# Kernel tuning notes

Hardware: AMD Instinct MI355X
Metric: run time of the kernel (lower is better)

Reference implementation:

```python
import jax, jax.numpy as jnp
import numpy as np

N_P, N_V, N_C, N_A = 8000, 3000, 1500, 6000
CLS = N_C
D = 128
E = 150000
N_TOT = N_P + N_V + N_C + N_A
LAMBDA1 = 1.0


def _cal_matrix(A):
    # row-normalize, leaving all-zero rows untouched (matches cal_matrix)
    d = jnp.sum(A, axis=1)
    safe = jnp.where(d > 0, d, 1.0)
    return jnp.where((d > 0)[:, None], A / safe[:, None], A)


def _linear(x, W, b):
    return x @ W.T + b


def _gru(x, h, Wih, Whh, bih, bhh):
    # torch.nn.GRUCell semantics; gate order r, z, n
    gi = x @ Wih.T + bih
    gh = h @ Whh.T + bhh
    ir, iz, inn = jnp.split(gi, 3, axis=1)
    hr, hz, hn = jnp.split(gh, 3, axis=1)
    r = jax.nn.sigmoid(ir + hr)
    z = jax.nn.sigmoid(iz + hz)
    n = jnp.tanh(inn + r * hn)
    return (1.0 - z) * n + z * h


def _ce_soft(pred, label):
    # torch CrossEntropyLoss with probabilistic targets; NOTE: pred is already
    # softmaxed in the original, so log_softmax is applied on top (faithful double softmax)
    return -jnp.mean(jnp.sum(label * jax.nn.log_softmax(pred, axis=1), axis=1))


def _fuse(e0, e1, W2, b2, W3, b3):
    # attention fusion: leaky_relu(., 0) == relu; softmax over the NODE axis (faithful)
    a = jnp.concatenate([_linear(e0, W2, b2), _linear(e1, W3, b3)], axis=0)  # [2N,1]
    alpha = jax.nn.softmax(jax.nn.relu(a).reshape(2, -1, 1), axis=1)
    return jax.nn.relu(jnp.sum(alpha * jnp.stack([e0, e1], axis=0), axis=0))


def _forward(feat_P, feat_V, feat_C, feat_A, W1, b1, W2, b2, W3, b3,
             L00W, L00b, L01W, L01b, L10W, L10b, L11W, L11b, L12W, L12b,
             g0_Wih, g0_Whh, g0_bih, g0_bhh, g1_Wih, g1_Whh, g1_bih, g1_bhh,
             rel_emb, adj00, adj01, adj10, adj11, adj12, clsA, clsP, clsV, u_s, u_d):
    # self embeddings via shared linear1
    self_P = _linear(feat_P, W1, b1)
    self_V = _linear(feat_V, W1, b1)
    self_C = _linear(feat_C, W1, b1)
    self_A = _linear(feat_A, W1, b1)
    loss_tcp = jnp.float32(0.0)
    # ---- meta-path 0: V -> P -> A (GRUCell 0) ----
    pred = jax.nn.softmax(_linear(feat_V, L00W, L00b), axis=1)        # [N_V, CLS]
    loss_tcp += _ce_soft(pred, clsV)
    tcp = jnp.sum(pred * clsV, axis=1, keepdims=True)                 # bmm([N,1,C],[N,C,1])
    h = adj00 @ (tcp * feat_V)                                        # [N_P, D]
    state_P0 = _gru(feat_P, h, g0_Wih, g0_Whh, g0_bih, g0_bhh)
    pred = jax.nn.softmax(_linear(state_P0, L01W, L01b), axis=1)
    loss_tcp += _ce_soft(pred, clsP)
    tcp = jnp.sum(pred * clsP, axis=1, keepdims=True)
    h = adj01 @ (tcp * state_P0)                                      # [N_A, D]
    state_A0 = _gru(feat_A, h, g0_Wih, g0_Whh, g0_bih, g0_bhh)
    # ---- meta-path 1: A -> P -> V -> C (GRUCell 1) ----
    pred = jax.nn.softmax(_linear(feat_A, L10W, L10b), axis=1)
    loss_tcp += _ce_soft(pred, clsA)
    tcp = jnp.sum(pred * clsA, axis=1, keepdims=True)
    h = adj10 @ (tcp * feat_A)                                        # [N_P, D]
    state_P1 = _gru(feat_P, h, g1_Wih, g1_Whh, g1_bih, g1_bhh)        # appended 3rd, unused by fusion
    pred = jax.nn.softmax(_linear(state_P1, L11W, L11b), axis=1)
    loss_tcp += _ce_soft(pred, clsP)
    tcp = jnp.sum(pred * clsP, axis=1, keepdims=True)
    h = adj11 @ (tcp * state_P1)                                      # [N_V, D]
    state_V1 = _gru(feat_V, h, g1_Wih, g1_Whh, g1_bih, g1_bhh)
    pred = jax.nn.softmax(_linear(state_V1, L12W, L12b), axis=1)
    loss_tcp += _ce_soft(pred, clsV)
    tcp = jnp.sum(pred * clsV, axis=1, keepdims=True)
    h = adj12 @ (tcp * state_V1)                                      # [N_C, D]
    state_C1 = _gru(feat_C, h, g1_Wih, g1_Whh, g1_bih, g1_bhh)
    # ---- attention fusion of (self_emb, first GRU state) per node type ----
    emb_P = _fuse(self_P, state_P0, W2, b2, W3, b3)
    emb_V = _fuse(self_V, state_V1, W2, b2, W3, b3)
    emb_C = _fuse(self_C, state_C1, W2, b2, W3, b3)
    emb_A = _fuse(self_A, state_A0, W2, b2, W3, b3)
    final_ent = jnp.concatenate([emb_P, emb_V, emb_C, emb_A], axis=0)  # order P,V,C,A
    # ---- link scoring ----
    lab_d = u_d[:, 2].astype(jnp.float32)
    lab_s = u_s[:, 2].astype(jnp.float32)
    M_r = rel_emb[u_d[:, 3]]
    inner_d = jnp.sum(M_r * jnp.tanh(final_ent[u_d[:, 0]] + final_ent[u_d[:, 1]]), axis=1)
    inner_s = jnp.sum(final_ent[u_s[:, 0]] * final_ent[u_s[:, 1]], axis=1)
    base = -jnp.sum(jax.nn.log_sigmoid(lab_d * inner_d)) - jnp.sum(jax.nn.log_sigmoid(lab_s * inner_s))
    # l2_loss_emb is 0 in the original; l2_loss is computed but never added to loss_emb
    loss = base + LAMBDA1 * loss_tcp
    return loss, final_ent, rel_emb


def setup_inputs():
    key = jax.random.key(0)
    ki = iter(jax.random.split(key, 48))
    def nk():
        return next(ki)
    def xav(o, i):  # xavier_normal_
        return jax.random.normal(nk(), (o, i), jnp.float32) * jnp.sqrt(2.0 / (o + i))
    def uni(shape):  # torch GRUCell default init
        k = 1.0 / float(np.sqrt(D))
        return jax.random.uniform(nk(), shape, jnp.float32, -k, k)
    def radj(o, i, p=0.003):  # raw binary adjacency
        return (jax.random.uniform(nk(), (o, i)) < p).astype(jnp.float32)

    feat_P = jax.random.normal(nk(), (N_P, D), jnp.float32)
    feat_V = jax.random.normal(nk(), (N_V, D), jnp.float32)
    feat_C = jax.random.normal(nk(), (N_C, D), jnp.float32)
    feat_A = jax.random.normal(nk(), (N_A, D), jnp.float32)
    A00 = radj(N_P, N_V); A01 = radj(N_A, N_P)
    A10 = radj(N_P, N_A); A11 = radj(N_V, N_P); A12 = radj(N_C, N_V)

    inp = dict(
        feat_P=feat_P, feat_V=feat_V, feat_C=feat_C, feat_A=feat_A,
        W1=xav(D, D), b1=jnp.zeros((D,), jnp.float32),
        W2=xav(1, D), b2=jnp.zeros((1,), jnp.float32),
        W3=xav(1, D), b3=jnp.zeros((1,), jnp.float32),
        L00W=xav(CLS, D), L00b=jnp.zeros((CLS,), jnp.float32),
        L01W=xav(CLS, D), L01b=jnp.zeros((CLS,), jnp.float32),
        L10W=xav(CLS, D), L10b=jnp.zeros((CLS,), jnp.float32),
        L11W=xav(CLS, D), L11b=jnp.zeros((CLS,), jnp.float32),
        L12W=xav(CLS, D), L12b=jnp.zeros((CLS,), jnp.float32),
        g0_Wih=uni((3 * D, D)), g0_Whh=uni((3 * D, D)), g0_bih=uni((3 * D,)), g0_bhh=uni((3 * D,)),
        g1_Wih=uni((3 * D, D)), g1_Whh=uni((3 * D, D)), g1_bih=uni((3 * D,)), g1_bhh=uni((3 * D,)),
        rel_emb=jax.random.normal(nk(), (12, D), jnp.float32),
        adj00=_cal_matrix(A00), adj01=_cal_matrix(A01),
        adj10=_cal_matrix(A10), adj11=_cal_matrix(A11), adj12=_cal_matrix(A12),
        clsA=_cal_matrix((A12 @ (A11 @ A10)).T),   # [N_A, CLS]
        clsP=_cal_matrix((A12 @ A11).T),           # [N_P, CLS]
        clsV=_cal_matrix(A12.T),                   # [N_V, CLS]
    )

    def edges(n_cols):
        i = jax.random.randint(nk(), (E,), 0, N_TOT)
        j = jax.random.randint(nk(), (E,), 0, N_TOT)
        lab = jax.random.randint(nk(), (E,), 0, 2) * 2 - 1  # labels in {-1,+1}
        cols = [i, j, lab]
        if n_cols == 4:
            cols.append(jax.random.randint(nk(), (E,), 0, 12))
        return jnp.stack(cols, axis=1)

    inp['u_s'] = edges(3)
    inp['u_d'] = edges(4)
    return inp


def reference(feat_P, feat_V, feat_C, feat_A, W1, b1, W2, b2, W3, b3,
              L00W, L00b, L01W, L01b, L10W, L10b, L11W, L11b, L12W, L12b,
              g0_Wih, g0_Whh, g0_bih, g0_bhh, g1_Wih, g1_Whh, g1_bih, g1_bhh,
              rel_emb, adj00, adj01, adj10, adj11, adj12, clsA, clsP, clsV, u_s, u_d):
    return _forward(feat_P, feat_V, feat_C, feat_A, W1, b1, W2, b2, W3, b3,
                    L00W, L00b, L01W, L01b, L10W, L10b, L11W, L11b, L12W, L12b,
                    g0_Wih, g0_Whh, g0_bih, g0_bhh, g1_Wih, g1_Whh, g1_bih, g1_bhh,
                    rel_emb, adj00, adj01, adj10, adj11, adj12, clsA, clsP, clsV, u_s, u_d)
```

## Files before the change

### kernel.cpp

```cpp
#include <hip/hip_runtime.h>
#include <cstdint>
#include <cstddef>

#define DEV_INLINE __device__ __forceinline__

typedef __attribute__((ext_vector_type(8))) short bf16x8;
typedef __attribute__((ext_vector_type(16))) float f32x16;
struct __align__(8) US4 { unsigned short u[4]; };

DEV_INLINE unsigned short f2bf(float x) {
  unsigned u = __float_as_uint(x);
  return (unsigned short)((u + 0x7FFFu + ((u >> 16) & 1u)) >> 16);
}
DEV_INLINE float2 bfpair(unsigned v) {
  return make_float2(__uint_as_float(v << 16), __uint_as_float(v & 0xFFFF0000u));
}

struct CvtSeg { const float* src; unsigned short* dst; int n; int nblk; };
struct CvtArgs { CvtSeg seg[16]; int nseg; };

__global__ __launch_bounds__(256) void convert_bf16_many(CvtArgs args) {
  int b = blockIdx.x;
  int s = 0;
  while (s < args.nseg && b >= args.seg[s].nblk) { b -= args.seg[s].nblk; ++s; }
  if (s >= args.nseg) return;
  int base = b * 1024 + threadIdx.x * 4;
  if (base >= args.seg[s].n) return;
  float4 v = *reinterpret_cast<const float4*>(args.seg[s].src + base);
  US4 o;
  o.u[0] = f2bf(v.x); o.u[1] = f2bf(v.y); o.u[2] = f2bf(v.z); o.u[3] = f2bf(v.w);
  *reinterpret_cast<US4*>(args.seg[s].dst + base) = o;
}

DEV_INLINE void gemm_body(
    const unsigned short* __restrict__ Xb, const unsigned short* __restrict__ Wb,
    const float* __restrict__ bias, float* __restrict__ C, int N, int O,
    int bm, int bn, unsigned short* Xs, unsigned short* Ws)
{
  const int tid = threadIdx.x;
#pragma unroll
  for (int i = 0; i < 8; ++i) {
    int s = tid + 256 * i;
    int row = s >> 4, c16 = s & 15;
    uint4 v = make_uint4(0, 0, 0, 0);
    int gr = bm + row;
    if (gr < N) v = *reinterpret_cast<const uint4*>(Xb + (size_t)gr * 128 + c16 * 8);
    *reinterpret_cast<uint4*>(&Xs[(row * 16 + (c16 ^ (row & 7))) * 8]) = v;
  }
#pragma unroll
  for (int i = 0; i < 4; ++i) {
    int s = tid + 256 * i;
    int row = s >> 4, c16 = s & 15;
    uint4 v = make_uint4(0, 0, 0, 0);
    int gw = bn + row;
    if (gw < O) v = *reinterpret_cast<const uint4*>(Wb + (size_t)gw * 128 + c16 * 8);
    *reinterpret_cast<uint4*>(&Ws[(row * 16 + (c16 ^ (row & 7))) * 8]) = v;
  }
  __syncthreads();

  const int wave = tid >> 6, lane = tid & 63;
  const int l31 = lane & 31, lhi = lane >> 5;

  f32x16 acc0, acc1;
#pragma unroll
  for (int i = 0; i < 16; ++i) { acc0[i] = 0.f; acc1[i] = 0.f; }

  const int ar = wave * 32 + l31;
#pragma unroll
  for (int ks = 0; ks < 8; ++ks) {
    int c16 = ks * 2 + lhi;
    bf16x8 a  = *reinterpret_cast<const bf16x8*>(&Xs[(ar * 16 + (c16 ^ (ar & 7))) * 8]);
    bf16x8 b0 = *reinterpret_cast<const bf16x8*>(&Ws[(l31 * 16 + (c16 ^ (l31 & 7))) * 8]);
    int br1 = 32 + l31;
    bf16x8 b1 = *reinterpret_cast<const bf16x8*>(&Ws[(br1 * 16 + (c16 ^ (br1 & 7))) * 8]);
    acc0 = __builtin_amdgcn_mfma_f32_32x32x16_bf16(a, b0, acc0, 0, 0, 0);
    acc1 = __builtin_amdgcn_mfma_f32_32x32x16_bf16(a, b1, acc1, 0, 0, 0);
  }

#pragma unroll
  for (int reg = 0; reg < 16; ++reg) {
    int r = bm + wave * 32 + (reg & 3) + 8 * (reg >> 2) + 4 * lhi;
    if (r < N) {
      int c0 = bn + l31;
      if (c0 < O) C[(size_t)r * O + c0] = acc0[reg] + bias[c0];
      int c1 = bn + 32 + l31;
      if (c1 < O) C[(size_t)r * O + c1] = acc1[reg] + bias[c1];
    }
  }
}

__global__ __launch_bounds__(256) void gemm_bf16(
    const unsigned short* __restrict__ Xb, const unsigned short* __restrict__ Wb,
    const float* __restrict__ bias, float* __restrict__ C, int N, int O)
{
  __shared__ __align__(16) unsigned short Xs[128 * 128];
  __shared__ __align__(16) unsigned short Ws[64 * 128];
  gemm_body(Xb, Wb, bias, C, N, O, blockIdx.x * 128, blockIdx.y * 64, Xs, Ws);
}

struct GSeg { const unsigned short* X; const unsigned short* W; const float* bias;
              float* C; int N; int O; int blk0; int xblk; };
struct GSegs { GSeg s[8]; int nseg; };

__global__ __launch_bounds__(256) void gemm_bf16_gseg(GSegs gs) {
  __shared__ __align__(16) unsigned short Xs[128 * 128];
  __shared__ __align__(16) unsigned short Ws[64 * 128];
  int bx = blockIdx.x;
  int si = 0;
  while (si + 1 < gs.nseg && bx >= gs.s[si + 1].blk0) ++si;
  const GSeg& g = gs.s[si];
  int b = bx - g.blk0;
  int bm = (b % g.xblk) * 128;
  int bn = (b / g.xblk) * 64;
  gemm_body(g.X, g.W, g.bias, g.C, g.N, g.O, bm, bn, Xs, Ws);
}

DEV_INLINE void ghgru_body(
    const unsigned short* __restrict__ Hb, const unsigned short* __restrict__ Whhb,
    const float* __restrict__ bhh, const float* __restrict__ gi,
    const float* __restrict__ hv, float* __restrict__ out,
    unsigned short* __restrict__ outb, int M, int bm, unsigned short* As)
{
  const int tid = threadIdx.x;
#pragma unroll
  for (int i = 0; i < 2; ++i) {
    int s = tid + 256 * i;
    int row = s >> 4, c16 = s & 15;
    uint4 v = make_uint4(0, 0, 0, 0);
    int gr = bm + row;
    if (gr < M) v = *reinterpret_cast<const uint4*>(Hb + (size_t)gr * 128 + c16 * 8);
    *reinterpret_cast<uint4*>(&As[(row * 16 + (c16 ^ (row & 7))) * 8]) = v;
  }
  __syncthreads();

  const int wave = tid >> 6, lane = tid & 63;
  const int l31 = lane & 31, lhi = lane >> 5;
  const int d = wave * 32 + l31;

  f32x16 ar, az, an;
#pragma unroll
  for (int i = 0; i < 16; ++i) { ar[i] = 0.f; az[i] = 0.f; an[i] = 0.f; }

#pragma unroll
  for (int ks = 0; ks < 8; ++ks) {
    int c16 = ks * 2 + lhi;
    bf16x8 a = *reinterpret_cast<const bf16x8*>(&As[(l31 * 16 + (c16 ^ (l31 & 7))) * 8]);
    const unsigned short* wb = Whhb + (size_t)c16 * 8;
    bf16x8 br = *reinterpret_cast<const bf16x8*>(wb + (size_t)d * 128);
    bf16x8 bz = *reinterpret_cast<const bf16x8*>(wb + (size_t)(128 + d) * 128);
    bf16x8 bn = *reinterpret_cast<const bf16x8*>(wb + (size_t)(256 + d) * 128);
    ar = __builtin_amdgcn_mfma_f32_32x32x16_bf16(a, br, ar, 0, 0, 0);
    az = __builtin_amdgcn_mfma_f32_32x32x16_bf16(a, bz, az, 0, 0, 0);
    an = __builtin_amdgcn_mfma_f32_32x32x16_bf16(a, bn, an, 0, 0, 0);
  }

  const float b_r = bhh[d], b_z = bhh[128 + d], b_n = bhh[256 + d];
#pragma unroll
  for (int reg = 0; reg < 16; ++reg) {
    int r = bm + (reg & 3) + 8 * (reg >> 2) + 4 * lhi;
    if (r < M) {
      const float* gir = gi + (size_t)r * 384;
      float rr = 1.f / (1.f + expf(-(gir[d] + ar[reg] + b_r)));
      float zz = 1.f / (1.f + expf(-(gir[128 + d] + az[reg] + b_z)));
      float nn = tanhf(gir[256 + d] + rr * (an[reg] + b_n));
      float h = hv[(size_t)r * 128 + d];
      float o = (1.f - zz) * nn + zz * h;
      out[(size_t)r * 128 + d] = o;
      outb[(size_t)r * 128 + d] = f2bf(o);
    }
  }
}

__global__ __launch_bounds__(256) void gh_gru(
    const unsigned short* __restrict__ Hb, const unsigned short* __restrict__ Whhb,
    const float* __restrict__ bhh, const float* __restrict__ gi,
    const float* __restrict__ hv, float* __restrict__ out,
    unsigned short* __restrict__ outb, int M)
{
  __shared__ __align__(16) unsigned short As[32 * 128];
  ghgru_body(Hb, Whhb, bhh, gi, hv, out, outb, M, blockIdx.x * 32, As);
}

__global__ __launch_bounds__(256) void gh_gru2(
    const unsigned short* Hb0, const unsigned short* Whh0, const float* bhh0,
    const float* gi0, const float* hv0, float* out0, unsigned short* outb0,
    int M0, int nblk0,
    const unsigned short* Hb1, const unsigned short* Whh1, const float* bhh1,
    const float* gi1, const float* hv1, float* out1, unsigned short* outb1, int M1)
{
  __shared__ __align__(16) unsigned short As[32 * 128];
  if ((int)blockIdx.x < nblk0)
    ghgru_body(Hb0, Whh0, bhh0, gi0, hv0, out0, outb0, M0, blockIdx.x * 32, As);
  else
    ghgru_body(Hb1, Whh1, bhh1, gi1, hv1, out1, outb1, M1, (blockIdx.x - nblk0) * 32, As);
}

DEV_INLINE void spmv_body(const float* __restrict__ A, const float* __restrict__ Xs,
                          float* __restrict__ H, unsigned short* __restrict__ Hb,
                          int row, int K, float (*red)[128])
{
  int tid = threadIdx.x, wave = tid >> 6, lane = tid & 63;
  const float4* Arow = reinterpret_cast<const float4*>(A + (size_t)row * K);
  int K4 = K >> 2;
  float acc0 = 0.f, acc1 = 0.f;
  for (int base = wave * 64; base < K4; base += 256) {
    int q = base + lane;
    float4 a = (q < K4) ? Arow[q] : make_float4(0.f, 0.f, 0.f, 0.f);
#pragma unroll
    for (int c = 0; c < 4; ++c) {
      float av = (c == 0) ? a.x : (c == 1) ? a.y : (c == 2) ? a.z : a.w;
      unsigned long long mm = __ballot(av != 0.f);
      while (mm) {
        int b = __builtin_ctzll(mm);
        mm &= mm - 1;
        float v = __shfl(av, b);
        int jj = (base + b) * 4 + c;
        const float* xr = Xs + (size_t)jj * 128;
        acc0 += v * xr[lane];
        acc1 += v * xr[lane + 64];
      }
    }
  }
  red[wave][lane] = acc0;
  red[wave][lane + 64] = acc1;
  __syncthreads();
  if (wave == 0) {
    float r0 = red[0][lane] + red[1][lane] + red[2][lane] + red[3][lane];
    float r1 = red[0][lane + 64] + red[1][lane + 64] + red[2][lane + 64] + red[3][lane + 64];
    H[(size_t)row * 128 + lane] = r0;
    H[(size_t)row * 128 + 64 + lane] = r1;
    Hb[(size_t)row * 128 + lane] = f2bf(r0);
    Hb[(size_t)row * 128 + 64 + lane] = f2bf(r1);
  }
}

__global__ __launch_bounds__(256) void spmv_scan(
    const float* __restrict__ A, const float* __restrict__ Xs,
    float* __restrict__ H, unsigned short* __restrict__ Hb, int M, int K)
{
  __shared__ float red[4][128];
  spmv_body(A, Xs, H, Hb, blockIdx.x, K, red);
}

__global__ __launch_bounds__(256) void spmv_scan2(
    const float* __restrict__ A0, const float* __restrict__ X0,
    float* __restrict__ H0, unsigned short* __restrict__ H0b, int M0, int K0,
    const float* __restrict__ A1, const float* __restrict__ X1,
    float* __restrict__ H1, unsigned short* __restrict__ H1b, int K1)
{
  __shared__ float red[4][128];
  if ((int)blockIdx.x < M0) spmv_body(A0, X0, H0, H0b, blockIdx.x, K0, red);
  else                      spmv_body(A1, X1, H1, H1b, blockIdx.x - M0, K1, red);
}

DEV_INLINE void rowops_body(int lane, const float4* __restrict__ lr,
                            const float4* __restrict__ cr,
                            const float* __restrict__ srcrow,
                            float* __restrict__ scaledrow, float* __restrict__ cep)
{
  float4 e[6];
  float m = -3.4e38f;
#pragma unroll
  for (int k = 0; k < 6; ++k) {
    int idx = k * 64 + lane;
    if (idx < 375) {
      e[k] = lr[idx];
      m = fmaxf(m, fmaxf(fmaxf(e[k].x, e[k].y), fmaxf(e[k].z, e[k].w)));
    } else {
      e[k] = make_float4(-3.4e38f, -3.4e38f, -3.4e38f, -3.4e38f);
    }
  }
#pragma unroll
  for (int o = 1; o < 64; o <<= 1) m = fmaxf(m, __shfl_xor(m, o));
  float z = 0.f;
#pragma unroll
  for (int k = 0; k < 6; ++k) {
    e[k].x = expf(e[k].x - m); e[k].y = expf(e[k].y - m);
    e[k].z = expf(e[k].z - m); e[k].w = expf(e[k].w - m);
    z += (e[k].x + e[k].y) + (e[k].z + e[k].w);
  }
#pragma unroll
  for (int o = 1; o < 64; o <<= 1) z += __shfl_xor(z, o);
  float invZ1 = 1.0f / z;
  float m2 = invZ1;
  float t = 0.f, ls = 0.f, z2 = 0.f;
#pragma unroll
  for (int k = 0; k < 6; ++k) {
    int idx = k * 64 + lane;
    if (idx < 375) {
      float4 c = cr[idx];
      float px = e[k].x * invZ1, py = e[k].y * invZ1;
      float pz = e[k].z * invZ1, pw = e[k].w * invZ1;
      t  += c.x * px + c.y * py + c.z * pz + c.w * pw;
      ls += (c.x + c.y) + (c.z + c.w);
      z2 += expf(px - m2) + expf(py - m2) + expf(pz - m2) + expf(pw - m2);
    }
  }
#pragma unroll
  for (int o = 1; o < 64; o <<= 1) {
    t += __shfl_xor(t, o); ls += __shfl_xor(ls, o); z2 += __shfl_xor(z2, o);
  }
  if (lane == 0) *cep = t - ls * (m2 + logf(z2));
  scaledrow[lane]      = t * srcrow[lane];
  scaledrow[lane + 64] = t * srcrow[lane + 64];
}

__global__ __launch_bounds__(256) void rowops_wave(
    const float* __restrict__ logits, const float* __restrict__ cls,
    const float* __restrict__ src, float* __restrict__ scaled,
    float* __restrict__ ce, int N)
{
  int gw = (blockIdx.x * 256 + threadIdx.x) >> 6;
  if (gw >= N) return;
  int lane = threadIdx.x & 63;
  rowops_body(lane,
              reinterpret_cast<const float4*>(logits + (size_t)gw * 1500),
              reinterpret_cast<const float4*>(cls + (size_t)gw * 1500),
              src + (size_t)gw * 128, scaled + (size_t)gw * 128, ce + gw);
}

__global__ __launch_bounds__(256) void rowops2(
    const float* lgA, const float* clsA_, const float* srcA, float* scA, float* ceA, int nA,
    const float* lgB, const float* clsB_, const float* srcB, float* scB, float* ceB, int nB)
{
  int gw = (blockIdx.x * 256 + threadIdx.x) >> 6;
  if (gw >= nA + nB) return;
  int lane = threadIdx.x & 63;
  if (gw < nA) {
    rowops_body(lane,
                reinterpret_cast<const float4*>(lgA + (size_t)gw * 1500),
                reinterpret_cast<const float4*>(clsA_ + (size_t)gw * 1500),
                srcA + (size_t)gw * 128, scA + (size_t)gw * 128, ceA + gw);
  } else {
    int r = gw - nA;
    rowops_body(lane,
                reinterpret_cast<const float4*>(lgB + (size_t)r * 1500),
                reinterpret_cast<const float4*>(clsB_ + (size_t)r * 1500),
                srcB + (size_t)r * 128, scB + (size_t)r * 128, ceB + r);
  }
}

__global__ __launch_bounds__(256) void fuse_scores_all(
    const float* __restrict__ e0, const float* __restrict__ e1,
    const float* __restrict__ W2, const float* __restrict__ b2,
    const float* __restrict__ W3, const float* __restrict__ b3,
    float* __restrict__ s0, float* __restrict__ s1)
{
  int lane = threadIdx.x & 63;
  int row = (blockIdx.x * 256 + threadIdx.x) >> 6;
  if (row >= 18500) return;
  float a0 = e0[(size_t)row * 128 + lane] * W2[lane] + e0[(size_t)row * 128 + 64 + lane] * W2[64 + lane];
  float a1 = e1[(size_t)row * 128 + lane] * W3[lane] + e1[(size_t)row * 128 + 64 + lane] * W3[64 + lane];
#pragma unroll
  for (int o = 32; o > 0; o >>= 1) { a0 += __shfl_down(a0, o); a1 += __shfl_down(a1, o); }
  if (lane == 0) {
    s0[row] = fmaxf(a0 + b2[0], 0.f);
    s1[row] = fmaxf(a1 + b3[0], 0.f);
  }
}

__global__ __launch_bounds__(1024) void denom4(
    const float* __restrict__ s0, const float* __restrict__ s1,
    float* __restrict__ den)
{
  __shared__ float red[1024];
  const int ns[4]   = {8000, 3000, 1500, 6000};
  const int offs[4] = {0, 8000, 11000, 12500};
  int b = blockIdx.x;
  int n = ns[b];
  const float* p0 = s0 + offs[b];
  const float* p1 = s1 + offs[b];
  int tid = threadIdx.x;
  float m = -3.4e38f;
  for (int i = tid; i < n; i += 1024) m = fmaxf(m, p0[i]);
  red[tid] = m; __syncthreads();
  for (int s = 512; s > 0; s >>= 1) { if (tid < s) red[tid] = fmaxf(red[tid], red[tid + s]); __syncthreads(); }
  float m0 = red[0]; __syncthreads();
  float z = 0.f;
  for (int i = tid; i < n; i += 1024) z += expf(p0[i] - m0);
  red[tid] = z; __syncthreads();
  for (int s = 512; s > 0; s >>= 1) { if (tid < s) red[tid] += red[tid + s]; __syncthreads(); }
  float Z0 = red[0]; __syncthreads();
  m = -3.4e38f;
  for (int i = tid; i < n; i += 1024) m = fmaxf(m, p1[i]);
  red[tid] = m; __syncthreads();
  for (int s = 512; s > 0; s >>= 1) { if (tid < s) red[tid] = fmaxf(red[tid], red[tid + s]); __syncthreads(); }
  float m1 = red[0]; __syncthreads();
  z = 0.f;
  for (int i = tid; i < n; i += 1024) z += expf(p1[i] - m1);
  red[tid] = z; __syncthreads();
  for (int s = 512; s > 0; s >>= 1) { if (tid < s) red[tid] += red[tid + s]; __syncthreads(); }
  if (tid == 0) { den[b * 4] = m0; den[b * 4 + 1] = Z0; den[b * 4 + 2] = m1; den[b * 4 + 3] = red[0]; }
}

__global__ __launch_bounds__(256) void fuse_emb_all(
    const float* __restrict__ e0, const float* __restrict__ e1,
    const float* __restrict__ s0, const float* __restrict__ s1,
    const float* __restrict__ den, const float* __restrict__ rel,
    float* __restrict__ fe, unsigned short* __restrict__ feb,
    float* __restrict__ rel_out)
{
  int t = blockIdx.x * 256 + threadIdx.x;
  const int tot2 = 18500 * 64;
  if (t < tot2) {
    int idx = t * 2;
    int row = idx >> 7;
    int e = (row < 8000) ? 0 : (row < 11000) ? 1 : (row < 12500) ? 2 : 3;
    float a0 = expf(s0[row] - den[e * 4]) / den[e * 4 + 1];
    float a1 = expf(s1[row] - den[e * 4 + 2]) / den[e * 4 + 3];
    float2 v0 = *reinterpret_cast<const float2*>(e0 + idx);
    float2 v1 = *reinterpret_cast<const float2*>(e1 + idx);
    float r0 = fmaxf(a0 * v0.x + a1 * v1.x, 0.f);
    float r1 = fmaxf(a0 * v0.y + a1 * v1.y, 0.f);
    *reinterpret_cast<float2*>(fe + idx) = make_float2(r0, r1);
    unsigned pb = (unsigned)f2bf(r0) | ((unsigned)f2bf(r1) << 16);
    *reinterpret_cast<unsigned*>(feb + idx) = pb;
  } else if (t < tot2 + 768) {
    int k = (t - tot2) * 2;
    *reinterpret_cast<float2*>(rel_out + k) = *reinterpret_cast<const float2*>(rel + k);
  }
}

__global__ __launch_bounds__(256) void edge_both(
    const int* __restrict__ ud, const int* __restrict__ us,
    const unsigned short* __restrict__ feb, const unsigned short* __restrict__ relb,
    float* __restrict__ partial, int En)
{
  int lane = threadIdx.x & 63;
  int wid = threadIdx.x >> 6;
  bool is_d = (blockIdx.x < 1024);
  int bb = is_d ? blockIdx.x : blockIdx.x - 1024;
  int gw = bb * 4 + wid;
  const int nw = 1024 * 4;
  float acc = 0.f;
  if (is_d) {
    for (int e = gw; e < En; e += nw) {
      int4 ei = *reinterpret_cast<const int4*>(ud + (size_t)e * 4);
      float2 fi = bfpair(reinterpret_cast<const unsigned*>(feb + (size_t)ei.x * 128)[lane]);
      float2 fj = bfpair(reinterpret_cast<const unsigned*>(feb + (size_t)ei.y * 128)[lane]);
      float2 rr = bfpair(reinterpret_cast<const unsigned*>(relb + (size_t)ei.w * 128)[lane]);
      float d = rr.x * tanhf(fi.x + fj.x) + rr.y * tanhf(fi.y + fj.y);
#pragma unroll
      for (int o = 32; o > 0; o >>= 1) d += __shfl_down(d, o);
      if (lane == 0) {
        float x = (float)ei.z * d;
        acc += (x >= 0.f) ? log1pf(expf(-x)) : (-x + log1pf(expf(x)));
      }
    }
  } else {
    for (int e = gw; e < En; e += nw) {
      int i = us[(size_t)e * 3], j = us[(size_t)e * 3 + 1], lab = us[(size_t)e * 3 + 2];
      float2 fi = bfpair(reinterpret_cast<const unsigned*>(feb + (size_t)i * 128)[lane]);
      float2 fj = bfpair(reinterpret_cast<const unsigned*>(feb + (size_t)j * 128)[lane]);
      float d = fi.x * fj.x + fi.y * fj.y;
#pragma unroll
      for (int o = 32; o > 0; o >>= 1) d += __shfl_down(d, o);
      if (lane == 0) {
        float x = (float)lab * d;
        acc += (x >= 0.f) ? log1pf(expf(-x)) : (-x + log1pf(expf(x)));
      }
    }
  }
  __shared__ float red[4];
  if (lane == 0) red[wid] = acc;
  __syncthreads();
  if (threadIdx.x == 0) partial[blockIdx.x] = red[0] + red[1] + red[2] + red[3];
}

__global__ __launch_bounds__(1024) void final_reduce(
    const float* __restrict__ partial, const float* __restrict__ cebuf,
    float* __restrict__ out)
{
  __shared__ float red[1024];
  __shared__ float total;
  int tid = threadIdx.x;
  if (tid == 0) total = 0.f;
  __syncthreads();
  float a = partial[tid] + partial[tid + 1024];
  red[tid] = a; __syncthreads();
  for (int s = 512; s > 0; s >>= 1) { if (tid < s) red[tid] += red[tid + s]; __syncthreads(); }
  if (tid == 0) total += red[0];
  __syncthreads();
  const int ns[5] = {3000, 8000, 6000, 8000, 3000};
#pragma unroll
  for (int seg = 0; seg < 5; ++seg) {
    const float* v = cebuf + seg * 8000;
    float s = 0.f;
    for (int i = tid; i < ns[seg]; i += 1024) s += v[i];
    red[tid] = s; __syncthreads();
    for (int st = 512; st > 0; st >>= 1) { if (tid < st) red[tid] += red[tid + st]; __syncthreads(); }
    if (tid == 0) total -= red[0] / (float)ns[seg];
    __syncthreads();
  }
  if (tid == 0) out[0] = total;
}

extern "C" void kernel_launch(void* const* d_in, const int* in_sizes, int n_in,
                              void* d_out, int out_size, void* d_ws, size_t ws_size,
                              hipStream_t stream)
{
  const float* feat_P = (const float*)d_in[0];
  const float* feat_V = (const float*)d_in[1];
  const float* feat_C = (const float*)d_in[2];
  const float* feat_A = (const float*)d_in[3];
  const float* W1 = (const float*)d_in[4];
  const float* b1 = (const float*)d_in[5];
  const float* W2 = (const float*)d_in[6];
  const float* b2 = (const float*)d_in[7];
  const float* W3 = (const float*)d_in[8];
  const float* b3 = (const float*)d_in[9];
  const float* L00W = (const float*)d_in[10];
  const float* L00b = (const float*)d_in[11];
  const float* L01W = (const float*)d_in[12];
  const float* L01b = (const float*)d_in[13];
  const float* L10W = (const float*)d_in[14];
  const float* L10b = (const float*)d_in[15];
  const float* L11W = (const float*)d_in[16];
  const float* L11b = (const float*)d_in[17];
  const float* L12W = (const float*)d_in[18];
  const float* L12b = (const float*)d_in[19];
  const float* g0_Wih = (const float*)d_in[20];
  const float* g0_Whh = (const float*)d_in[21];
  const float* g0_bih = (const float*)d_in[22];
  const float* g0_bhh = (const float*)d_in[23];
  const float* g1_Wih = (const float*)d_in[24];
  const float* g1_Whh = (const float*)d_in[25];
  const float* g1_bih = (const float*)d_in[26];
  const float* g1_bhh = (const float*)d_in[27];
  const float* rel_emb = (const float*)d_in[28];
  const float* adj00 = (const float*)d_in[29];
  const float* adj01 = (const float*)d_in[30];
  const float* adj10 = (const float*)d_in[31];
  const float* adj11 = (const float*)d_in[32];
  const float* adj12 = (const float*)d_in[33];
  const float* clsA = (const float*)d_in[34];
  const float* clsP = (const float*)d_in[35];
  const float* clsV = (const float*)d_in[36];
  const int* u_s = (const int*)d_in[37];
  const int* u_d = (const int*)d_in[38];

  float* out = (float*)d_out;
  float* fe = out + 1;
  float* rel_out = out + 1 + 18500 * 128;

  float* ws = (float*)d_ws;
  size_t o = 0;
  auto alloc = [&](size_t n) { float* p = ws + o; o += n; return p; };
  float* selfb   = alloc((size_t)18500 * 128);
  float* stcat   = alloc((size_t)18500 * 128);
  float* stP1    = alloc((size_t)8000 * 128);
  float* gi      = alloc((size_t)26500 * 384);
  float* logits  = alloc((size_t)8000 * 1500);
  float* logits0 = alloc((size_t)3000 * 1500);
  float* logits2 = alloc((size_t)8000 * 1500);
  float* scaled1 = alloc((size_t)8000 * 128);
  float* scaled3 = alloc((size_t)8000 * 128);
  float* scaled0 = alloc((size_t)3000 * 128);
  float* scaled2 = alloc((size_t)6000 * 128);
  float* scaled4 = alloc((size_t)3000 * 128);
  float* h0      = alloc((size_t)8000 * 128);
  float* h2      = alloc((size_t)8000 * 128);
  float* h1      = alloc((size_t)6000 * 128);
  float* h3      = alloc((size_t)3000 * 128);
  float* h4      = alloc((size_t)1500 * 128);
  float* cebuf   = alloc(5 * 8000);
  float* s0b = alloc(18500);
  float* s1b = alloc(18500);
  float* den = alloc(16);
  float* partial = alloc(2048);
  auto allocb = [&](size_t nelem) { unsigned short* p = (unsigned short*)(ws + o); o += (nelem + 1) / 2; return p; };
  unsigned short* featb  = allocb((size_t)18500 * 128);
  unsigned short* stcatb = allocb((size_t)18500 * 128);
  unsigned short* stP1b  = allocb((size_t)8000 * 128);
  unsigned short* feb    = allocb((size_t)18500 * 128);
  unsigned short* h0b    = allocb((size_t)8000 * 128);
  unsigned short* h2b    = allocb((size_t)8000 * 128);
  unsigned short* h1b    = allocb((size_t)6000 * 128);
  unsigned short* h3b    = allocb((size_t)3000 * 128);
  unsigned short* h4b    = allocb((size_t)1500 * 128);
  unsigned short* relb   = allocb(12 * 128);
  unsigned short* W1b = allocb(128 * 128);
  unsigned short* L00Wb = allocb(1500 * 128);
  unsigned short* L01Wb = allocb(1500 * 128);
  unsigned short* L10Wb = allocb(1500 * 128);
  unsigned short* L11Wb = allocb(1500 * 128);
  unsigned short* L12Wb = allocb(1500 * 128);
  unsigned short* g0Wihb = allocb(384 * 128);
  unsigned short* g0Whhb = allocb(384 * 128);
  unsigned short* g1Wihb = allocb(384 * 128);
  unsigned short* g1Whhb = allocb(384 * 128);
  unsigned short* featPb = featb;
  unsigned short* featVb = featb + (size_t)8000 * 128;
  unsigned short* featCb = featb + (size_t)11000 * 128;
  unsigned short* featAb = featb + (size_t)12500 * 128;
  float* stP0 = stcat;
  float* stV1 = stcat + (size_t)8000 * 128;
  float* stC1 = stcat + (size_t)11000 * 128;
  float* stA0 = stcat + (size_t)12500 * 128;
  unsigned short* stP0b = stcatb;
  unsigned short* stV1b = stcatb + (size_t)8000 * 128;
  unsigned short* stC1b = stcatb + (size_t)11000 * 128;
  unsigned short* stA0b = stcatb + (size_t)12500 * 128;
  (void)ws_size; (void)in_sizes; (void)n_in; (void)out_size;

  dim3 blk(256);

  CvtArgs ca{};
  int nseg = 0, totblk = 0;
  auto addseg = [&](const float* src, unsigned short* dst, int n) {
    ca.seg[nseg].src = src; ca.seg[nseg].dst = dst; ca.seg[nseg].n = n;
    ca.seg[nseg].nblk = (n + 1023) / 1024; totblk += ca.seg[nseg].nblk; ++nseg;
  };
  addseg(feat_P, featPb, 8000 * 128);
  addseg(feat_V, featVb, 3000 * 128);
  addseg(feat_C, featCb, 1500 * 128);
  addseg(feat_A, featAb, 6000 * 128);
  addseg(W1, W1b, 128 * 128);
  addseg(L00W, L00Wb, 1500 * 128);
  addseg(L01W, L01Wb, 1500 * 128);
  addseg(L10W, L10Wb, 1500 * 128);
  addseg(L11W, L11Wb, 1500 * 128);
  addseg(L12W, L12Wb, 1500 * 128);
  addseg(g0_Wih, g0Wihb, 384 * 128);
  addseg(g0_Whh, g0Whhb, 384 * 128);
  addseg(g1_Wih, g1Wihb, 384 * 128);
  addseg(g1_Whh, g1Whhb, 384 * 128);
  addseg(rel_emb, relb, 12 * 128);
  ca.nseg = nseg;
  hipLaunchKernelGGL(convert_bf16_many, dim3(totblk), blk, 0, stream, ca);

  const size_t giOff[5] = {0, 8000, 14000, 22000, 25000};

  {
    GSegs gs{};
    int nb = 0, k = 0;
    auto add = [&](const unsigned short* X, const unsigned short* W, const float* bias,
                   float* C, int N, int O) {
      int xb = (N + 127) / 128, yb = (O + 63) / 64;
      gs.s[k] = GSeg{X, W, bias, C, N, O, nb, xb};
      nb += xb * yb; ++k;
    };
    add(featb,  W1b,    b1,     selfb,             18500, 128);
    add(featPb, g0Wihb, g0_bih, gi + giOff[0] * 384, 8000, 384);
    add(featAb, g0Wihb, g0_bih, gi + giOff[1] * 384, 6000, 384);
    add(featPb, g1Wihb, g1_bih, gi + giOff[2] * 384, 8000, 384);
    add(featVb, g1Wihb, g1_bih, gi + giOff[3] * 384, 3000, 384);
    add(featCb, g1Wihb, g1_bih, gi + giOff[4] * 384, 1500, 384);
    add(featVb, L00Wb,  L00b,   logits0,            3000, 1500);
    add(featAb, L10Wb,  L10b,   logits2,            6000, 1500);
    gs.nseg = k;
    hipLaunchKernelGGL(gemm_bf16_gseg, dim3(nb), blk, 0, stream, gs);
  }

  hipLaunchKernelGGL(rowops2, dim3((9000 * 64 + 255) / 256), blk, 0, stream,
                     logits0, clsV, feat_V, scaled0, cebuf + 0 * 8000, 3000,
                     logits2, clsA, feat_A, scaled2, cebuf + 2 * 8000, 6000);
  hipLaunchKernelGGL(spmv_scan2, dim3(16000), blk, 0, stream,
                     adj00, scaled0, h0, h0b, 8000, 3000,
                     adj10, scaled2, h2, h2b, 6000);
  hipLaunchKernelGGL(gh_gru2, dim3(500), blk, 0, stream,
                     h0b, g0Whhb, g0_bhh, gi + giOff[0] * 384, h0, stP0, stP0b, 8000, 250,
                     h2b, g1Whhb, g1_bhh, gi + giOff[2] * 384, h2, stP1, stP1b, 8000);
  {
    GSegs gs{};
    gs.s[0] = GSeg{stP0b, L01Wb, L01b, logits,  8000, 1500, 0,    63};
    gs.s[1] = GSeg{stP1b, L11Wb, L11b, logits2, 8000, 1500, 1512, 63};
    gs.nseg = 2;
    hipLaunchKernelGGL(gemm_bf16_gseg, dim3(3024), blk, 0, stream, gs);
  }
  hipLaunchKernelGGL(rowops2, dim3((16000 * 64 + 255) / 256), blk, 0, stream,
                     logits,  clsP, stP0, scaled1, cebuf + 1 * 8000, 8000,
                     logits2, clsP, stP1, scaled3, cebuf + 3 * 8000, 8000);
  hipLaunchKernelGGL(spmv_scan2, dim3(9000), blk, 0, stream,
                     adj01, scaled1, h1, h1b, 6000, 8000,
                     adj11, scaled3, h3, h3b, 8000);
  hipLaunchKernelGGL(gh_gru2, dim3(188 + 94), blk, 0, stream,
                     h1b, g0Whhb, g0_bhh, gi + giOff[1] * 384, h1, stA0, stA0b, 6000, 188,
                     h3b, g1Whhb, g1_bhh, gi + giOff[3] * 384, h3, stV1, stV1b, 3000);
  hipLaunchKernelGGL(gemm_bf16, dim3(24, 24), blk, 0, stream, stV1b, L12Wb, L12b, logits, 3000, 1500);
  hipLaunchKernelGGL(rowops_wave, dim3((3000 * 64 + 255) / 256), blk, 0, stream,
                     logits, clsV, stV1, scaled4, cebuf + 4 * 8000, 3000);
  hipLaunchKernelGGL(spmv_scan, dim3(1500), blk, 0, stream, adj12, scaled4, h4, h4b, 1500, 3000);
  hipLaunchKernelGGL(gh_gru, dim3(47), blk, 0, stream,
                     h4b, g1Whhb, g1_bhh, gi + giOff[4] * 384, h4, stC1, stC1b, 1500);

  hipLaunchKernelGGL(fuse_scores_all, dim3((18500 + 3) / 4), blk, 0, stream,
                     selfb, stcat, W2, b2, W3, b3, s0b, s1b);
  hipLaunchKernelGGL(denom4, dim3(4), dim3(1024), 0, stream, s0b, s1b, den);
  hipLaunchKernelGGL(fuse_emb_all, dim3((18500 * 64 + 768 + 255) / 256), blk, 0, stream,
                     selfb, stcat, s0b, s1b, den, rel_emb, fe, feb, rel_out);

  hipLaunchKernelGGL(edge_both, dim3(2048), blk, 0, stream, u_d, u_s, feb, relb, partial, 150000);

  hipLaunchKernelGGL(final_reduce, dim3(1), dim3(1024), 0, stream, partial, cebuf, out);
}
```

Before: 555.4 us.

## Emit bf16 logits, fast exp, prefetch spmv rows, fuse final reduce

The second-hop classifier GEMMs now write bf16 logits instead of fp32, and new rowops kernels read them packed, halving logits write and read traffic. Precise expf is replaced by __expf in the GRU, softmax and loss paths. The spmv loop prefetches the next adjacency float4 before processing the current one. The final reduction is folded into the edge kernel through a last-block atomic counter, removing one launch. Risks are the lower precision of bf16 logits and fast exp, plus correctness of the counter, which appears to be reset inside fuse_emb_all.

```diff
diff --git a/kernel.cpp b/kernel.cpp
--- a/kernel.cpp
+++ b/kernel.cpp
@@ -32,10 +32,10 @@
   *reinterpret_cast<US4*>(args.seg[s].dst + base) = o;
 }
 
-DEV_INLINE void gemm_body(
-    const unsigned short* __restrict__ Xb, const unsigned short* __restrict__ Wb,
-    const float* __restrict__ bias, float* __restrict__ C, int N, int O,
-    int bm, int bn, unsigned short* Xs, unsigned short* Ws)
+DEV_INLINE void gemm_stage(const unsigned short* __restrict__ Xb,
+                           const unsigned short* __restrict__ Wb,
+                           int N, int O, int bm, int bn,
+                           unsigned short* Xs, unsigned short* Ws)
 {
   const int tid = threadIdx.x;
 #pragma unroll
@@ -57,14 +57,16 @@
     *reinterpret_cast<uint4*>(&Ws[(row * 16 + (c16 ^ (row & 7))) * 8]) = v;
   }
   __syncthreads();
-
+}
+
+DEV_INLINE void gemm_mfma(const unsigned short* Xs, const unsigned short* Ws,
+                          f32x16& acc0, f32x16& acc1)
+{
+  const int tid = threadIdx.x;
   const int wave = tid >> 6, lane = tid & 63;
   const int l31 = lane & 31, lhi = lane >> 5;
-
-  f32x16 acc0, acc1;
 #pragma unroll
   for (int i = 0; i < 16; ++i) { acc0[i] = 0.f; acc1[i] = 0.f; }
-
   const int ar = wave * 32 + l31;
 #pragma unroll
   for (int ks = 0; ks < 8; ++ks) {
@@ -76,7 +78,19 @@
     acc0 = __builtin_amdgcn_mfma_f32_32x32x16_bf16(a, b0, acc0, 0, 0, 0);
     acc1 = __builtin_amdgcn_mfma_f32_32x32x16_bf16(a, b1, acc1, 0, 0, 0);
   }
-
+}
+
+DEV_INLINE void gemm_body(
+    const unsigned short* __restrict__ Xb, const unsigned short* __restrict__ Wb,
+    const float* __restrict__ bias, float* __restrict__ C, int N, int O,
+    int bm, int bn, unsigned short* Xs, unsigned short* Ws)
+{
+  gemm_stage(Xb, Wb, N, O, bm, bn, Xs, Ws);
+  const int tid = threadIdx.x;
+  const int wave = tid >> 6, lane = tid & 63;
+  const int l31 = lane & 31, lhi = lane >> 5;
+  f32x16 acc0, acc1;
+  gemm_mfma(Xs, Ws, acc0, acc1);
 #pragma unroll
   for (int reg = 0; reg < 16; ++reg) {
     int r = bm + wave * 32 + (reg & 3) + 8 * (reg >> 2) + 4 * lhi;
@@ -89,13 +103,27 @@
   }
 }
 
-__global__ __launch_bounds__(256) void gemm_bf16(
+DEV_INLINE void gemm_body_b(
     const unsigned short* __restrict__ Xb, const unsigned short* __restrict__ Wb,
-    const float* __restrict__ bias, float* __restrict__ C, int N, int O)
-{
-  __shared__ __align__(16) unsigned short Xs[128 * 128];
-  __shared__ __align__(16) unsigned short Ws[64 * 128];
-  gemm_body(Xb, Wb, bias, C, N, O, blockIdx.x * 128, blockIdx.y * 64, Xs, Ws);
+    const float* __restrict__ bias, unsigned short* __restrict__ Cb, int N, int O,
+    int bm, int bn, unsigned short* Xs, unsigned short* Ws)
+{
+  gemm_stage(Xb, Wb, N, O, bm, bn, Xs, Ws);
+  const int tid = threadIdx.x;
+  const int wave = tid >> 6, lane = tid & 63;
+  const int l31 = lane & 31, lhi = lane >> 5;
+  f32x16 acc0, acc1;
+  gemm_mfma(Xs, Ws, acc0, acc1);
+#pragma unroll
+  for (int reg = 0; reg < 16; ++reg) {
+    int r = bm + wave * 32 + (reg & 3) + 8 * (reg >> 2) + 4 * lhi;
+    if (r < N) {
+      int c0 = bn + l31;
+      if (c0 < O) Cb[(size_t)r * O + c0] = f2bf(acc0[reg] + bias[c0]);
+      int c1 = bn + 32 + l31;
+      if (c1 < O) Cb[(size_t)r * O + c1] = f2bf(acc1[reg] + bias[c1]);
+    }
+  }
 }
 
 struct GSeg { const unsigned short* X; const unsigned short* W; const float* bias;
@@ -110,89 +138,22 @@
   while (si + 1 < gs.nseg && bx >= gs.s[si + 1].blk0) ++si;
   const GSeg& g = gs.s[si];
   int b = bx - g.blk0;
-  int bm = (b % g.xblk) * 128;
-  int bn = (b / g.xblk) * 64;
-  gemm_body(g.X, g.W, g.bias, g.C, g.N, g.O, bm, bn, Xs, Ws);
-}
-
-DEV_INLINE void ghgru_body(
-    const unsigned short* __restrict__ Hb, const unsigned short* __restrict__ Whhb,
-    const float* __restrict__ bhh, const float* __restrict__ gi,
-    const float* __restrict__ hv, float* __restrict__ out,
-    unsigned short* __restrict__ outb, int M, int bm, unsigned short* As)
-{
-  const int tid = threadIdx.x;
-#pragma unroll
-  for (int i = 0; i < 2; ++i) {
-    int s = tid + 256 * i;
-    int row = s >> 4, c16 = s & 15;
-    uint4 v = make_uint4(0, 0, 0, 0);
-    int gr = bm + row;
-    if (gr < M) v = *reinterpret_cast<const uint4*>(Hb + (size_t)gr * 128 + c16 * 8);
-    *reinterpret_cast<uint4*>(&As[(row * 16 + (c16 ^ (row & 7))) * 8]) = v;
-  }
-  __syncthreads();
-
-  const int wave = tid >> 6, lane = tid & 63;
-  const int l31 = lane & 31, lhi = lane >> 5;
-  const int d = wave * 32 + l31;
-
-  f32x16 ar, az, an;
-#pragma unroll
-  for (int i = 0; i < 16; ++i) { ar[i] = 0.f; az[i] = 0.f; an[i] = 0.f; }
-
-#pragma unroll
-  for (int ks = 0; ks < 8; ++ks) {
-    int c16 = ks * 2 + lhi;
-    bf16x8 a = *reinterpret_cast<const bf16x8*>(&As[(l31 * 16 + (c16 ^ (l31 & 7))) * 8]);
-    const unsigned short* wb = Whhb + (size_t)c16 * 8;
-    bf16x8 br = *reinterpret_cast<const bf16x8*>(wb + (size_t)d * 128);
-    bf16x8 bz = *reinterpret_cast<const bf16x8*>(wb + (size_t)(128 + d) * 128);
-    bf16x8 bn = *reinterpret_cast<const bf16x8*>(wb + (size_t)(256 + d) * 128);
-    ar = __builtin_amdgcn_mfma_f32_32x32x16_bf16(a, br, ar, 0, 0, 0);
-    az = __builtin_amdgcn_mfma_f32_32x32x16_bf16(a, bz, az, 0, 0, 0);
-    an = __builtin_amdgcn_mfma_f32_32x32x16_bf16(a, bn, an, 0, 0, 0);
-  }
-
-  const float b_r = bhh[d], b_z = bhh[128 + d], b_n = bhh[256 + d];
-#pragma unroll
-  for (int reg = 0; reg < 16; ++reg) {
-    int r = bm + (reg & 3) + 8 * (reg >> 2) + 4 * lhi;
-    if (r < M) {
-      const float* gir = gi + (size_t)r * 384;
-      float rr = 1.f / (1.f + expf(-(gir[d] + ar[reg] + b_r)));
-      float zz = 1.f / (1.f + expf(-(gir[128 + d] + az[reg] + b_z)));
-      float nn = tanhf(gir[256 + d] + rr * (an[reg] + b_n));
-      float h = hv[(size_t)r * 128 + d];
-      float o = (1.f - zz) * nn + zz * h;
-      out[(size_t)r * 128 + d] = o;
-      outb[(size_t)r * 128 + d] = f2bf(o);
-    }
-  }
-}
-
-__global__ __launch_bounds__(256) void gh_gru(
-    const unsigned short* __restrict__ Hb, const unsigned short* __restrict__ Whhb,
-    const float* __restrict__ bhh, const float* __restrict__ gi,
-    const float* __restrict__ hv, float* __restrict__ out,
-    unsigned short* __restrict__ outb, int M)
-{
-  __shared__ __align__(16) unsigned short As[32 * 128];
-  ghgru_body(Hb, Whhb, bhh, gi, hv, out, outb, M, blockIdx.x * 32, As);
-}
-
-__global__ __launch_bounds__(256) void gh_gru2(
-    const unsigned short* Hb0, const unsigned short* Whh0, const float* bhh0,
-    const float* gi0, const float* hv0, float* out0, unsigned short* outb0,
-    int M0, int nblk0,
-    const unsigned short* Hb1, const unsigned short* Whh1, const float* bhh1,
-    const float* gi1, const float* hv1, float* out1, unsigned short* outb1, int M1)
-{
-  __shared__ __align__(16) unsigned short As[32 * 128];
-  if ((int)blockIdx.x < nblk0)
-    ghgru_body(Hb0, Whh0, bhh0, gi0, hv0, out0, outb0, M0, blockIdx.x * 32, As);
-  else
-    ghgru_body(Hb1, Whh1, bhh1, gi1, hv1, out1, outb1, M1, (blockIdx.x - nblk0) * 32, As);
+  gemm_body(g.X, g.W, g.bias, g.C, g.N, g.O, (b % g.xblk) * 128, (b / g.xblk) * 64, Xs, Ws);
+}
+
+struct GBSeg { const unsigned short* X; const unsigned short* W; const float* bias;
+               unsigned short* C; int N; int O; int blk0; int xblk; };
+struct GBSegs { GBSeg s[4]; int nseg; };
+
+__global__ __launch_bounds__(256) void gemm_bf16o_gseg(GBSegs gs) {
+  __shared__ __align__(16) unsigned short Xs[128 * 128];
+  __shared__ __align__(16) unsigned short Ws[64 * 128];
+  int bx = blockIdx.x;
+  int si = 0;
+  while (si + 1 < gs.nseg && bx >= gs.s[si + 1].blk0) ++si;
+  const GBSeg& g = gs.s[si];
+  int b = bx - g.blk0;
+  gemm_body_b(g.X, g.W, g.bias, g.C, g.N, g.O, (b % g.xblk) * 128, (b / g.xblk) * 64, Xs, Ws);
 }
 
 DEV_INLINE void spmv_body(const float* __restrict__ A, const float* __restrict__ Xs,
@@ -203,9 +164,13 @@
   const float4* Arow = reinterpret_cast<const float4*>(A + (size_t)row * K);
   int K4 = K >> 2;
   float acc0 = 0.f, acc1 = 0.f;
-  for (int base = wave * 64; base < K4; base += 256) {
-    int q = base + lane;
-    float4 a = (q < K4) ? Arow[q] : make_float4(0.f, 0.f, 0.f, 0.f);
+  int base = wave * 64;
+  int q = base + lane;
+  float4 a = (base < K4 && q < K4) ? Arow[q] : make_float4(0.f, 0.f, 0.f, 0.f);
+  for (; base < K4; base += 256) {
+    int nb = base + 256;
+    int nq = nb + lane;
+    float4 an = (nb < K4 && nq < K4) ? Arow[nq] : make_float4(0.f, 0.f, 0.f, 0.f);
 #pragma unroll
     for (int c = 0; c < 4; ++c) {
       float av = (c == 0) ? a.x : (c == 1) ? a.y : (c == 2) ? a.z : a.w;
@@ -220,6 +185,7 @@
         acc1 += v * xr[lane + 64];
       }
     }
+    a = an;
   }
   red[wave][lane] = acc0;
   red[wave][lane + 64] = acc1;
@@ -253,6 +219,86 @@
   else                      spmv_body(A1, X1, H1, H1b, blockIdx.x - M0, K1, red);
 }
 
+DEV_INLINE void ghgru_body(
+    const unsigned short* __restrict__ Hb, const unsigned short* __restrict__ Whhb,
+    const float* __restrict__ bhh, const float* __restrict__ gi,
+    const float* __restrict__ hv, float* __restrict__ out,
+    unsigned short* __restrict__ outb, int M, int bm, unsigned short* As)
+{
+  const int tid = threadIdx.x;
+#pragma unroll
+  for (int i = 0; i < 2; ++i) {
+    int s = tid + 256 * i;
+    int row = s >> 4, c16 = s & 15;
+    uint4 v = make_uint4(0, 0, 0, 0);
+    int gr = bm + row;
+    if (gr < M) v = *reinterpret_cast<const uint4*>(Hb + (size_t)gr * 128 + c16 * 8);
+    *reinterpret_cast<uint4*>(&As[(row * 16 + (c16 ^ (row & 7))) * 8]) = v;
+  }
+  __syncthreads();
+
+  const int wave = tid >> 6, lane = tid & 63;
+  const int l31 = lane & 31, lhi = lane >> 5;
+  const int d = wave * 32 + l31;
+
+  f32x16 ar, az, an;
+#pragma unroll
+  for (int i = 0; i < 16; ++i) { ar[i] = 0.f; az[i] = 0.f; an[i] = 0.f; }
+
+#pragma unroll
+  for (int ks = 0; ks < 8; ++ks) {
+    int c16 = ks * 2 + lhi;
+    bf16x8 a = *reinterpret_cast<const bf16x8*>(&As[(l31 * 16 + (c16 ^ (l31 & 7))) * 8]);
+    const unsigned short* wb = Whhb + (size_t)c16 * 8;
+    bf16x8 br = *reinterpret_cast<const bf16x8*>(wb + (size_t)d * 128);
+    bf16x8 bz = *reinterpret_cast<const bf16x8*>(wb + (size_t)(128 + d) * 128);
+    bf16x8 bn = *reinterpret_cast<const bf16x8*>(wb + (size_t)(256 + d) * 128);
+    ar = __builtin_amdgcn_mfma_f32_32x32x16_bf16(a, br, ar, 0, 0, 0);
+    az = __builtin_amdgcn_mfma_f32_32x32x16_bf16(a, bz, az, 0, 0, 0);
+    an = __builtin_amdgcn_mfma_f32_32x32x16_bf16(a, bn, an, 0, 0, 0);
+  }
+
+  const float b_r = bhh[d], b_z = bhh[128 + d], b_n = bhh[256 + d];
+#pragma unroll
+  for (int reg = 0; reg < 16; ++reg) {
+    int r = bm + (reg & 3) + 8 * (reg >> 2) + 4 * lhi;
+    if (r < M) {
+      const float* gir = gi + (size_t)r * 384;
+      float rr = 1.f / (1.f + __expf(-(gir[d] + ar[reg] + b_r)));
+      float zz = 1.f / (1.f + __expf(-(gir[128 + d] + az[reg] + b_z)));
+      float nn = tanhf(gir[256 + d] + rr * (an[reg] + b_n));
+      float h = hv[(size_t)r * 128 + d];
+      float o = (1.f - zz) * nn + zz * h;
+      out[(size_t)r * 128 + d] = o;
+      outb[(size_t)r * 128 + d] = f2bf(o);
+    }
+  }
+}
+
+__global__ __launch_bounds__(256) void gh_gru(
+    const unsigned short* __restrict__ Hb, const unsigned short* __restrict__ Whhb,
+    const float* __restrict__ bhh, const float* __restrict__ gi,
+    const float* __restrict__ hv, float* __restrict__ out,
+    unsigned short* __restrict__ outb, int M)
+{
+  __shared__ __align__(16) unsigned short As[32 * 128];
+  ghgru_body(Hb, Whhb, bhh, gi, hv, out, outb, M, blockIdx.x * 32, As);
+}
+
+__global__ __launch_bounds__(256) void gh_gru2(
+    const unsigned short* Hb0, const unsigned short* Whh0, const float* bhh0,
+    const float* gi0, const float* hv0, float* out0, unsigned short* outb0,
+    int M0, int nblk0,
+    const unsigned short* Hb1, const unsigned short* Whh1, const float* bhh1,
+    const float* gi1, const float* hv1, float* out1, unsigned short* outb1, int M1)
+{
+  __shared__ __align__(16) unsigned short As[32 * 128];
+  if ((int)blockIdx.x < nblk0)
+    ghgru_body(Hb0, Whh0, bhh0, gi0, hv0, out0, outb0, M0, blockIdx.x * 32, As);
+  else
+    ghgru_body(Hb1, Whh1, bhh1, gi1, hv1, out1, outb1, M1, (blockIdx.x - nblk0) * 32, As);
+}
+
 DEV_INLINE void rowops_body(int lane, const float4* __restrict__ lr,
                             const float4* __restrict__ cr,
                             const float* __restrict__ srcrow,
@@ -275,8 +321,8 @@
   float z = 0.f;
 #pragma unroll
   for (int k = 0; k < 6; ++k) {
-    e[k].x = expf(e[k].x - m); e[k].y = expf(e[k].y - m);
-    e[k].z = expf(e[k].z - m); e[k].w = expf(e[k].w - m);
+    e[k].x = __expf(e[k].x - m); e[k].y = __expf(e[k].y - m);
+    e[k].z = __expf(e[k].z - m); e[k].w = __expf(e[k].w - m);
     z += (e[k].x + e[k].y) + (e[k].z + e[k].w);
   }
 #pragma unroll
@@ -293,7 +339,7 @@
       float pz = e[k].z * invZ1, pw = e[k].w * invZ1;
       t  += c.x * px + c.y * py + c.z * pz + c.w * pw;
       ls += (c.x + c.y) + (c.z + c.w);
-      z2 += expf(px - m2) + expf(py - m2) + expf(pz - m2) + expf(pw - m2);
+      z2 += __expf(px - m2) + __expf(py - m2) + __expf(pz - m2) + __expf(pw - m2);
     }
   }
 #pragma unroll
@@ -303,20 +349,6 @@
   if (lane == 0) *cep = t - ls * (m2 + logf(z2));
   scaledrow[lane]      = t * srcrow[lane];
   scaledrow[lane + 64] = t * srcrow[lane + 64];
-}
-
-__global__ __launch_bounds__(256) void rowops_wave(
-    const float* __restrict__ logits, const float* __restrict__ cls,
-    const float* __restrict__ src, float* __restrict__ scaled,
-    float* __restrict__ ce, int N)
-{
-  int gw = (blockIdx.x * 256 + threadIdx.x) >> 6;
-  if (gw >= N) return;
-  int lane = threadIdx.x & 63;
-  rowops_body(lane,
-              reinterpret_cast<const float4*>(logits + (size_t)gw * 1500),
-              reinterpret_cast<const float4*>(cls + (size_t)gw * 1500),
-              src + (size_t)gw * 128, scaled + (size_t)gw * 128, ce + gw);
 }
 
 __global__ __launch_bounds__(256) void rowops2(
@@ -340,6 +372,86 @@
   }
 }
 
+DEV_INLINE void rowops_body_b(int lane, const unsigned* __restrict__ lrb,
+                              const float2* __restrict__ cr2,
+                              const float* __restrict__ srcrow,
+                              float* __restrict__ scaledrow, float* __restrict__ cep)
+{
+  float2 e[12];
+  float m = -3.4e38f;
+#pragma unroll
+  for (int k = 0; k < 12; ++k) {
+    int idx = k * 64 + lane;
+    if (idx < 750) {
+      e[k] = bfpair(lrb[idx]);
+      m = fmaxf(m, fmaxf(e[k].x, e[k].y));
+    } else {
+      e[k] = make_float2(-3.4e38f, -3.4e38f);
+    }
+  }
+#pragma unroll
+  for (int o = 1; o < 64; o <<= 1) m = fmaxf(m, __shfl_xor(m, o));
+  float z = 0.f;
+#pragma unroll
+  for (int k = 0; k < 12; ++k) {
+    e[k].x = __expf(e[k].x - m); e[k].y = __expf(e[k].y - m);
+    z += e[k].x + e[k].y;
+  }
+#pragma unroll
+  for (int o = 1; o < 64; o <<= 1) z += __shfl_xor(z, o);
+  float invZ1 = 1.0f / z;
+  float m2 = invZ1;
+  float t = 0.f, ls = 0.f, z2 = 0.f;
+#pragma unroll
+  for (int k = 0; k < 12; ++k) {
+    int idx = k * 64 + lane;
+    if (idx < 750) {
+      float2 c = cr2[idx];
+      float px = e[k].x * invZ1, py = e[k].y * invZ1;
+      t  += c.x * px + c.y * py;
+      ls += c.x + c.y;
+      z2 += __expf(px - m2) + __expf(py - m2);
+    }
+  }
+#pragma unroll
+  for (int o = 1; o < 64; o <<= 1) {
+    t += __shfl_xor(t, o); ls += __shfl_xor(ls, o); z2 += __shfl_xor(z2, o);
+  }
+  if (lane == 0) *cep = t - ls * (m2 + logf(z2));
+  scaledrow[lane]      = t * srcrow[lane];
+  scaledrow[lane + 64] = t * srcrow[lane + 64];
+}
+
+__global__ __launch_bounds__(256) void rowops2b(
+    const unsigned* lgA, const float* clsA_, const float* srcA, float* scA, float* ceA, int nA,
+    const unsigned* lgB, const float* clsB_, const float* srcB, float* scB, float* ceB, int nB)
+{
+  int gw = (blockIdx.x * 256 + threadIdx.x) >> 6;
+  if (gw >= nA + nB) return;
+  int lane = threadIdx.x & 63;
+  if (gw < nA) {
+    rowops_body_b(lane, lgA + (size_t)gw * 750,
+                  reinterpret_cast<const float2*>(clsA_ + (size_t)gw * 1500),
+                  srcA + (size_t)gw * 128, scA + (size_t)gw * 128, ceA + gw);
+  } else {
+    int r = gw - nA;
+    rowops_body_b(lane, lgB + (size_t)r * 750,
+                  reinterpret_cast<const float2*>(clsB_ + (size_t)r * 1500),
+                  srcB + (size_t)r * 128, scB + (size_t)r * 128, ceB + r);
+  }
+}
+
+__global__ __launch_bounds__(256) void rowops1b(
+    const unsigned* lg, const float* cls, const float* src, float* sc, float* ce, int n)
+{
+  int gw = (blockIdx.x * 256 + threadIdx.x) >> 6;
+  if (gw >= n) return;
+  int lane = threadIdx.x & 63;
+  rowops_body_b(lane, lg + (size_t)gw * 750,
+                reinterpret_cast<const float2*>(cls + (size_t)gw * 1500),
+                src + (size_t)gw * 128, sc + (size_t)gw * 128, ce + gw);
+}
+
 __global__ __launch_bounds__(256) void fuse_scores_all(
     const float* __restrict__ e0, const float* __restrict__ e1,
     const float* __restrict__ W2, const float* __restrict__ b2,
@@ -377,7 +489,7 @@
   for (int s = 512; s > 0; s >>= 1) { if (tid < s) red[tid] = fmaxf(red[tid], red[tid + s]); __syncthreads(); }
   float m0 = red[0]; __syncthreads();
   float z = 0.f;
-  for (int i = tid; i < n; i += 1024) z += expf(p0[i] - m0);
+  for (int i = tid; i < n; i += 1024) z += __expf(p0[i] - m0);
   red[tid] = z; __syncthreads();
   for (int s = 512; s > 0; s >>= 1) { if (tid < s) red[tid] += red[tid + s]; __syncthreads(); }
   float Z0 = red[0]; __syncthreads();
@@ -387,7 +499,7 @@
   for (int s = 512; s > 0; s >>= 1) { if (tid < s) red[tid] = fmaxf(red[tid], red[tid + s]); __syncthreads(); }
   float m1 = red[0]; __syncthreads();
   z = 0.f;
-  for (int i = tid; i < n; i += 1024) z += expf(p1[i] - m1);
+  for (int i = tid; i < n; i += 1024) z += __expf(p1[i] - m1);
   red[tid] = z; __syncthreads();
   for (int s = 512; s > 0; s >>= 1) { if (tid < s) red[tid] += red[tid + s]; __syncthreads(); }
   if (tid == 0) { den[b * 4] = m0; den[b * 4 + 1] = Z0; den[b * 4 + 2] = m1; den[b * 4 + 3] = red[0]; }
@@ -398,16 +510,17 @@
     const float* __restrict__ s0, const float* __restrict__ s1,
     const float* __restrict__ den, const float* __restrict__ rel,
     float* __restrict__ fe, unsigned short* __restrict__ feb,
-    float* __restrict__ rel_out)
+    float* __restrict__ rel_out, unsigned* __restrict__ ctr)
 {
   int t = blockIdx.x * 256 + threadIdx.x;
+  if (t == 0) *ctr = 0;
   const int tot2 = 18500 * 64;
   if (t < tot2) {
     int idx = t * 2;
     int row = idx >> 7;
     int e = (row < 8000) ? 0 : (row < 11000) ? 1 : (row < 12500) ? 2 : 3;
-    float a0 = expf(s0[row] - den[e * 4]) / den[e * 4 + 1];
-    float a1 = expf(s1[row] - den[e * 4 + 2]) / den[e * 4 + 3];
+    float a0 = __expf(s0[row] - den[e * 4]) / den[e * 4 + 1];
+    float a1 = __expf(s1[row] - den[e * 4 + 2]) / den[e * 4 + 3];
     float2 v0 = *reinterpret_cast<const float2*>(e0 + idx);
     float2 v1 = *reinterpret_cast<const float2*>(e1 + idx);
     float r0 = fmaxf(a0 * v0.x + a1 * v1.x, 0.f);
@@ -421,10 +534,12 @@
   }
 }
 
-__global__ __launch_bounds__(256) void edge_both(
+__global__ __launch_bounds__(256) void edge_both_final(
     const int* __restrict__ ud, const int* __restrict__ us,
     const unsigned short* __restrict__ feb, const unsigned short* __restrict__ relb,
-    float* __restrict__ partial, int En)
+    float* __restrict__ partial, int En,
+    const float* __restrict__ cebuf, unsigned* __restrict__ ctr,
+    float* __restrict__ out)
 {
   int lane = threadIdx.x & 63;
   int wid = threadIdx.x >> 6;
@@ -444,7 +559,7 @@
       for (int o = 32; o > 0; o >>= 1) d += __shfl_down(d, o);
       if (lane == 0) {
         float x = (float)ei.z * d;
-        acc += (x >= 0.f) ? log1pf(expf(-x)) : (-x + log1pf(expf(x)));
+        acc += (x >= 0.f) ? log1pf(__expf(-x)) : (-x + log1pf(__expf(x)));
       }
     }
   } else {
@@ -457,42 +572,42 @@
       for (int o = 32; o > 0; o >>= 1) d += __shfl_down(d, o);
       if (lane == 0) {
         float x = (float)lab * d;
-        acc += (x >= 0.f) ? log1pf(expf(-x)) : (-x + log1pf(expf(x)));
+        acc += (x >= 0.f) ? log1pf(__expf(-x)) : (-x + log1pf(__expf(x)));
       }
     }
   }
   __shared__ float red[4];
   if (lane == 0) red[wid] = acc;
   __syncthreads();
-  if (threadIdx.x == 0) partial[blockIdx.x] = red[0] + red[1] + red[2] + red[3];
-}
-
-__global__ __launch_bounds__(1024) void final_reduce(
-    const float* __restrict__ partial, const float* __restrict__ cebuf,
-    float* __restrict__ out)
-{
-  __shared__ float red[1024];
-  __shared__ float total;
-  int tid = threadIdx.x;
-  if (tid == 0) total = 0.f;
+  __shared__ unsigned myturn;
+  if (threadIdx.x == 0) {
+    partial[blockIdx.x] = red[0] + red[1] + red[2] + red[3];
+    __threadfence();
+    myturn = atomicAdd(ctr, 1u);
+  }
   __syncthreads();
-  float a = partial[tid] + partial[tid + 1024];
-  red[tid] = a; __syncthreads();
-  for (int s = 512; s > 0; s >>= 1) { if (tid < s) red[tid] += red[tid + s]; __syncthreads(); }
-  if (tid == 0) total += red[0];
-  __syncthreads();
-  const int ns[5] = {3000, 8000, 6000, 8000, 3000};
-#pragma unroll
-  for (int seg = 0; seg < 5; ++seg) {
-    const float* v = cebuf + seg * 8000;
-    float s = 0.f;
-    for (int i = tid; i < ns[seg]; i += 1024) s += v[i];
-    red[tid] = s; __syncthreads();
-    for (int st = 512; st > 0; st >>= 1) { if (tid < st) red[tid] += red[tid + st]; __syncthreads(); }
-    if (tid == 0) total -= red[0] / (float)ns[seg];
-    __syncthreads();
-  }
-  if (tid == 0) out[0] = total;
+  if (myturn == 2047) {
+    __threadfence();
+    __shared__ float red2[256];
+    int tid = threadIdx.x;
+    float a = 0.f;
+    for (int i = tid; i < 2048; i += 256) a += partial[i];
+    red2[tid] = a; __syncthreads();
+    for (int s = 128; s > 0; s >>= 1) { if (tid < s) red2[tid] += red2[tid + s]; __syncthreads(); }
+    float total = red2[0]; __syncthreads();
+    const int ns[5] = {3000, 8000, 6000, 8000, 3000};
+#pragma unroll
+    for (int seg = 0; seg < 5; ++seg) {
+      const float* v = cebuf + seg * 8000;
+      float s = 0.f;
+      for (int i = tid; i < ns[seg]; i += 256) s += v[i];
+      red2[tid] = s; __syncthreads();
+      for (int st = 128; st > 0; st >>= 1) { if (tid < st) red2[tid] += red2[tid + st]; __syncthreads(); }
+      if (tid == 0) total -= red2[0] / (float)ns[seg];
+      __syncthreads();
+    }
+    if (tid == 0) out[0] = total;
+  }
 }
 
 extern "C" void kernel_launch(void* const* d_in, const int* in_sizes, int n_in,
@@ -550,13 +665,12 @@
   float* stcat   = alloc((size_t)18500 * 128);
   float* stP1    = alloc((size_t)8000 * 128);
   float* gi      = alloc((size_t)26500 * 384);
-  float* logits  = alloc((size_t)8000 * 1500);
   float* logits0 = alloc((size_t)3000 * 1500);
-  float* logits2 = alloc((size_t)8000 * 1500);
+  float* logits2 = alloc((size_t)6000 * 1500);
+  float* scaled0 = alloc((size_t)3000 * 128);
   float* scaled1 = alloc((size_t)8000 * 128);
+  float* scaled2 = alloc((size_t)6000 * 128);
   float* scaled3 = alloc((size_t)8000 * 128);
-  float* scaled0 = alloc((size_t)3000 * 128);
-  float* scaled2 = alloc((size_t)6000 * 128);
   float* scaled4 = alloc((size_t)3000 * 128);
   float* h0      = alloc((size_t)8000 * 128);
   float* h2      = alloc((size_t)8000 * 128);
@@ -568,6 +682,7 @@
   float* s1b = alloc(18500);
   float* den = alloc(16);
   float* partial = alloc(2048);
+  unsigned* ctr = (unsigned*)alloc(4);
   auto allocb = [&](size_t nelem) { unsigned short* p = (unsigned short*)(ws + o); o += (nelem + 1) / 2; return p; };
   unsigned short* featb  = allocb((size_t)18500 * 128);
   unsigned short* stcatb = allocb((size_t)18500 * 128);
@@ -578,6 +693,8 @@
   unsigned short* h1b    = allocb((size_t)6000 * 128);
   unsigned short* h3b    = allocb((size_t)3000 * 128);
   unsigned short* h4b    = allocb((size_t)1500 * 128);
+  unsigned short* lg1b   = allocb((size_t)8000 * 1500);
+  unsigned short* lg3b   = allocb((size_t)8000 * 1500);
   unsigned short* relb   = allocb(12 * 128);
   unsigned short* W1b = allocb(128 * 128);
   unsigned short* L00Wb = allocb(1500 * 128);
@@ -640,14 +757,14 @@
       gs.s[k] = GSeg{X, W, bias, C, N, O, nb, xb};
       nb += xb * yb; ++k;
     };
-    add(featb,  W1b,    b1,     selfb,             18500, 128);
+    add(featb,  W1b,    b1,     selfb,               18500, 128);
     add(featPb, g0Wihb, g0_bih, gi + giOff[0] * 384, 8000, 384);
     add(featAb, g0Wihb, g0_bih, gi + giOff[1] * 384, 6000, 384);
     add(featPb, g1Wihb, g1_bih, gi + giOff[2] * 384, 8000, 384);
     add(featVb, g1Wihb, g1_bih, gi + giOff[3] * 384, 3000, 384);
     add(featCb, g1Wihb, g1_bih, gi + giOff[4] * 384, 1500, 384);
-    add(featVb, L00Wb,  L00b,   logits0,            3000, 1500);
-    add(featAb, L10Wb,  L10b,   logits2,            6000, 1500);
+    add(featVb, L00Wb,  L00b,   logits0,             3000, 1500);
+    add(featAb, L10Wb,  L10b,   logits2,             6000, 1500);
     gs.nseg = k;
     hipLaunchKernelGGL(gemm_bf16_gseg, dim3(nb), blk, 0, stream, gs);
   }
@@ -662,24 +779,29 @@
                      h0b, g0Whhb, g0_bhh, gi + giOff[0] * 384, h0, stP0, stP0b, 8000, 250,
                      h2b, g1Whhb, g1_bhh, gi + giOff[2] * 384, h2, stP1, stP1b, 8000);
   {
-    GSegs gs{};
-    gs.s[0] = GSeg{stP0b, L01Wb, L01b, logits,  8000, 1500, 0,    63};
-    gs.s[1] = GSeg{stP1b, L11Wb, L11b, logits2, 8000, 1500, 1512, 63};
+    GBSegs gs{};
+    gs.s[0] = GBSeg{stP0b, L01Wb, L01b, lg1b, 8000, 1500, 0,    63};
+    gs.s[1] = GBSeg{stP1b, L11Wb, L11b, lg3b, 8000, 1500, 1512, 63};
     gs.nseg = 2;
-    hipLaunchKernelGGL(gemm_bf16_gseg, dim3(3024), blk, 0, stream, gs);
-  }
-  hipLaunchKernelGGL(rowops2, dim3((16000 * 64 + 255) / 256), blk, 0, stream,
-                     logits,  clsP, stP0, scaled1, cebuf + 1 * 8000, 8000,
-                     logits2, clsP, stP1, scaled3, cebuf + 3 * 8000, 8000);
+    hipLaunchKernelGGL(gemm_bf16o_gseg, dim3(3024), blk, 0, stream, gs);
+  }
+  hipLaunchKernelGGL(rowops2b, dim3((16000 * 64 + 255) / 256), blk, 0, stream,
+                     (const unsigned*)lg1b, clsP, stP0, scaled1, cebuf + 1 * 8000, 8000,
+                     (const unsigned*)lg3b, clsP, stP1, scaled3, cebuf + 3 * 8000, 8000);
   hipLaunchKernelGGL(spmv_scan2, dim3(9000), blk, 0, stream,
                      adj01, scaled1, h1, h1b, 6000, 8000,
                      adj11, scaled3, h3, h3b, 8000);
   hipLaunchKernelGGL(gh_gru2, dim3(188 + 94), blk, 0, stream,
                      h1b, g0Whhb, g0_bhh, gi + giOff[1] * 384, h1, stA0, stA0b, 6000, 188,
                      h3b, g1Whhb, g1_bhh, gi + giOff[3] * 384, h3, stV1, stV1b, 3000);
-  hipLaunchKernelGGL(gemm_bf16, dim3(24, 24), blk, 0, stream, stV1b, L12Wb, L12b, logits, 3000, 1500);
-  hipLaunchKernelGGL(rowops_wave, dim3((3000 * 64 + 255) / 256), blk, 0, stream,
-                     logits, clsV, stV1, scaled4, cebuf + 4 * 8000, 3000);
+  {
+    GBSegs gs{};
+    gs.s[0] = GBSeg{stV1b, L12Wb, L12b, lg1b, 3000, 1500, 0, 24};
+    gs.nseg = 1;
+    hipLaunchKernelGGL(gemm_bf16o_gseg, dim3(24 * 24), blk, 0, stream, gs);
+  }
+  hipLaunchKernelGGL(rowops1b, dim3((3000 * 64 + 255) / 256), blk, 0, stream,
+                     (const unsigned*)lg1b, clsV, stV1, scaled4, cebuf + 4 * 8000, 3000);
   hipLaunchKernelGGL(spmv_scan, dim3(1500), blk, 0, stream, adj12, scaled4, h4, h4b, 1500, 3000);
   hipLaunchKernelGGL(gh_gru, dim3(47), blk, 0, stream,
                      h4b, g1Whhb, g1_bhh, gi + giOff[4] * 384, h4, stC1, stC1b, 1500);
@@ -688,9 +810,8 @@
                      selfb, stcat, W2, b2, W3, b3, s0b, s1b);
   hipLaunchKernelGGL(denom4, dim3(4), dim3(1024), 0, stream, s0b, s1b, den);
   hipLaunchKernelGGL(fuse_emb_all, dim3((18500 * 64 + 768 + 255) / 256), blk, 0, stream,
-                     selfb, stcat, s0b, s1b, den, rel_emb, fe, feb, rel_out);
-
-  hipLaunchKernelGGL(edge_both, dim3(2048), blk, 0, stream, u_d, u_s, feb, relb, partial, 150000);
-
-  hipLaunchKernelGGL(final_reduce, dim3(1), dim3(1024), 0, stream, partial, cebuf, out);
-}
+                     selfb, stcat, s0b, s1b, den, rel_emb, fe, feb, rel_out, ctr);
+
+  hipLaunchKernelGGL(edge_both_final, dim3(2048), blk, 0, stream,
+                     u_d, u_s, feb, relb, partial, 150000, cebuf, ctr, out);
+}
```

New measurement: 603.2 us. +8.6%, slower.
